# Performance work log

Hardware: AMD Instinct MI355X
Metric: run time of the kernel (lower is better)

## Reference

```python
import jax, jax.numpy as jnp
import numpy as np

V, SMAX, D, H, L, DFF, W = 32000, 1024, 1024, 16, 2, 4096, 256
HD = D // H
EPS = 1e-6


def setup_inputs() -> dict:
    key = jax.random.key(0)
    ks = jax.random.split(key, 20)
    s = lambda k, shape, scale=0.02: jax.random.normal(k, shape, dtype=jnp.float32) * scale
    return {
        "input_ids": jax.random.randint(ks[0], (2, SMAX), 0, V, dtype=jnp.int64),
        "emb": s(ks[1], (V, D)),
        "pos": s(ks[2], (SMAX, D)),
        "norm1_w": jnp.ones((L, D), jnp.float32),
        "norm2_w": jnp.ones((L, D), jnp.float32),
        "wq": s(ks[3], (L, D, D)), "bq": jnp.zeros((L, D), jnp.float32),
        "wk": s(ks[4], (L, D, D)), "bk": jnp.zeros((L, D), jnp.float32),
        "wv": s(ks[5], (L, D, D)), "bv": jnp.zeros((L, D), jnp.float32),
        "wo": s(ks[6], (L, D, D)), "bo": jnp.zeros((L, D), jnp.float32),
        "w1": s(ks[7], (L, D, DFF)), "b1": jnp.zeros((L, DFF), jnp.float32),
        "w2": s(ks[8], (L, DFF, D)), "b2": jnp.zeros((L, D), jnp.float32),
        "normf_w": jnp.ones((D,), jnp.float32),
    }


def rms(x, w):
    return x * jax.lax.rsqrt(jnp.mean(x * x, axis=-1, keepdims=True) + EPS) * w


def reference(input_ids, emb, pos, norm1_w, norm2_w, wq, bq, wk, bk, wv, bv,
              wo, bo, w1, b1, w2, b2, normf_w):
    B, S = input_ids.shape
    x = emb[input_ids] + pos[:S]  # [B,S,D]
    # sliding-window causal mask: attend to j with 0 <= i-j < W
    i = jnp.arange(S)[:, None]
    j = jnp.arange(S)[None, :]
    mask = (j <= i) & (i - j < W)  # [S,S]
    neg = jnp.asarray(-1e9, x.dtype)
    for l in range(L):
        h = rms(x, norm1_w[l])
        q = (h @ wq[l] + bq[l]).reshape(B, S, H, HD)
        k = (h @ wk[l] + bk[l]).reshape(B, S, H, HD)
        v = (h @ wv[l] + bv[l]).reshape(B, S, H, HD)
        scores = jnp.einsum('bqhd,bkhd->bhqk', q, k) / np.sqrt(HD).astype(np.float32)
        scores = jnp.where(mask[None, None], scores, neg)
        attn = jax.nn.softmax(scores, axis=-1)
        o = jnp.einsum('bhqk,bkhd->bqhd', attn, v).reshape(B, S, D)
        x = x + (o @ wo[l] + bo[l])
        h2 = rms(x, norm2_w[l])
        x = x + (jax.nn.gelu(h2 @ w1[l] + b1[l], approximate=False) @ w2[l] + b2[l])
    x = rms(x, normf_w)
    logits = x @ emb.T  # tied lm_head
    return logits
```

## Files before the change

kernel.cpp:

```cpp
#include <hip/hip_runtime.h>
#include <hip/hip_bf16.h>
#include <cstdint>

typedef __bf16 bf16;
typedef __bf16 bf16x8 __attribute__((ext_vector_type(8)));
typedef __bf16 bf16x4 __attribute__((ext_vector_type(4)));
typedef float  f32x4  __attribute__((ext_vector_type(4)));

constexpr int V_    = 32000;
constexpr int SMAX_ = 1024;
constexpr int D_    = 1024;
constexpr int H_    = 16;
constexpr int L_    = 2;
constexpr int DFF_  = 4096;
constexpr int WIN_  = 256;
constexpr int B_    = 2;
constexpr int M_    = B_ * SMAX_;

#define SBAR0_() __builtin_amdgcn_sched_barrier(0)
#define HWBAR_() { __builtin_amdgcn_s_barrier(); SBAR0_(); }
#define LGKM0_() { asm volatile("s_waitcnt lgkmcnt(0)" ::: "memory"); SBAR0_(); }
#define VM0_()   { asm volatile("s_waitcnt vmcnt(0)" ::: "memory"); SBAR0_(); }

__global__ __launch_bounds__(512, 1) void gemm_lm3(
    const bf16* __restrict__ A, const bf16* __restrict__ BT,
    float* __restrict__ outf, int Nn)
{
  constexpr int KK = 1024, NT = 16;
  __shared__ __align__(16) bf16 ldsA[2][16384];
  __shared__ __align__(16) bf16 ldsB[2][16384];

  const int t = threadIdx.x, lane = t & 63, w = t >> 6;
  const int l16 = lane & 15, lh = lane >> 4;
  const int wm = w >> 2, wn = w & 3;

  const int nloc = gridDim.x >> 3;
  const int wg = (blockIdx.x & 7) * nloc + (blockIdx.x >> 3);
  const long m0 = (long)(wg & 7) * 256;
  const long n0 = (long)(wg >> 3) * 256;

  auto STGA = [&](int c, int k0) {
    #pragma unroll
    for (int q = 0; q < 4; ++q) {
      int row = q * 64 + (t >> 3);
      int sl  = (t & 7) ^ (row & 7);
      const bf16* g = A + (m0 + row) * (long)KK + k0 + sl * 8;
      __builtin_amdgcn_global_load_lds(
          (const __attribute__((address_space(1))) uint32_t*)g,
          (__attribute__((address_space(3))) uint32_t*)(&ldsA[c][q * 4096 + t * 8]),
          16, 0, 0);
    }
  };
  auto STGB = [&](int c, int k0) {
    #pragma unroll
    for (int q = 0; q < 4; ++q) {
      int row = q * 64 + (t >> 3);
      int sl  = (t & 7) ^ (row & 7);
      const bf16* g = BT + (n0 + row) * (long)KK + k0 + sl * 8;
      __builtin_amdgcn_global_load_lds(
          (const __attribute__((address_space(1))) uint32_t*)g,
          (__attribute__((address_space(3))) uint32_t*)(&ldsB[c][q * 4096 + t * 8]),
          16, 0, 0);
    }
  };
  auto LDA = [&](int c, int mi, int ks) -> bf16x8 {
    int row = wm * 128 + mi * 16 + l16;
    int sl  = (ks * 4 + lh) ^ (row & 7);
    return *(const bf16x8*)(&ldsA[c][row * 64 + sl * 8]);
  };
  auto LDB = [&](int c, int ni, int ks) -> bf16x8 {
    int row = wn * 64 + ni * 16 + l16;
    int sl  = (ks * 4 + lh) ^ (row & 7);
    return *(const bf16x8*)(&ldsB[c][row * 64 + sl * 8]);
  };

  f32x4 acc[8][4] = {};
  bf16x8 a[8], b[4];

  STGA(0, 0); STGB(0, 0);
  int kNext = 64;

  for (int j = 0; j < NT; ++j) {
    const int c = j & 1;
    VM0_();
    HWBAR_();
    #pragma unroll
    for (int mi = 0; mi < 8; ++mi) a[mi] = LDA(c, mi, 0);
    #pragma unroll
    for (int ni = 0; ni < 4; ++ni) b[ni] = LDB(c, ni, 0);
    STGA(c ^ 1, kNext); STGB(c ^ 1, kNext);
    LGKM0_();
    __builtin_amdgcn_s_setprio(1);
    #pragma unroll
    for (int mi = 0; mi < 8; ++mi)
      #pragma unroll
      for (int ni = 0; ni < 4; ++ni)
        acc[mi][ni] = __builtin_amdgcn_mfma_f32_16x16x32_bf16(a[mi], b[ni], acc[mi][ni], 0, 0, 0);
    __builtin_amdgcn_s_setprio(0);
    HWBAR_();
    #pragma unroll
    for (int mi = 0; mi < 8; ++mi) a[mi] = LDA(c, mi, 1);
    #pragma unroll
    for (int ni = 0; ni < 4; ++ni) b[ni] = LDB(c, ni, 1);
    LGKM0_();
    __builtin_amdgcn_s_setprio(1);
    #pragma unroll
    for (int mi = 0; mi < 8; ++mi)
      #pragma unroll
      for (int ni = 0; ni < 4; ++ni)
        acc[mi][ni] = __builtin_amdgcn_mfma_f32_16x16x32_bf16(a[mi], b[ni], acc[mi][ni], 0, 0, 0);
    __builtin_amdgcn_s_setprio(0);
    kNext += 64; if (kNext == KK) kNext = 0;
  }

  asm volatile("s_waitcnt vmcnt(0) lgkmcnt(0)" ::: "memory");
  #pragma unroll
  for (int mi = 0; mi < 8; ++mi)
    #pragma unroll
    for (int ni = 0; ni < 4; ++ni)
      #pragma unroll
      for (int rr = 0; rr < 4; ++rr) {
        long row = m0 + wm * 128 + mi * 16 + lh * 4 + rr;
        long col = n0 + wn * 64 + ni * 16 + l16;
        outf[row * Nn + col] = acc[mi][ni][rr];
      }
}

template<int BM, int EPI>
__global__ __launch_bounds__(256) void gemm_l2(
    const bf16* __restrict__ A, const bf16* __restrict__ BT,
    const float* __restrict__ bias, float* __restrict__ resid,
    bf16* __restrict__ outb, float* __restrict__ outf,
    int Nn, int Kk, int nbyMask, int nbyShift)
{
  constexpr int MR = BM / 32;
  constexpr int CA = BM / 32;
  __shared__ __align__(16) bf16 ldsA[2][BM * 64];
  __shared__ __align__(16) bf16 ldsB[2][8192];

  const int t = threadIdx.x, lane = t & 63, w = t >> 6;
  const int l16 = lane & 15, lh = lane >> 4;
  const int wm = w >> 1, wn = w & 1;

  const int nwg = gridDim.x, bid = blockIdx.x;
  const int nloc = nwg >> 3;
  const int wg = (bid & 7) * nloc + (bid >> 3);
  const long m0 = (long)(wg & nbyMask) * BM;
  const long n0 = (long)(wg >> nbyShift) * 128;

  auto STGA = [&](int c, int k0) {
    #pragma unroll
    for (int q = 0; q < CA; ++q) {
      int row = q * 32 + (t >> 3);
      int sl  = (t & 7) ^ (row & 7);
      const bf16* g = A + (m0 + row) * (long)Kk + k0 + sl * 8;
      __builtin_amdgcn_global_load_lds(
          (const __attribute__((address_space(1))) uint32_t*)g,
          (__attribute__((address_space(3))) uint32_t*)(&ldsA[c][q * 2048 + t * 8]),
          16, 0, 0);
    }
  };
  auto STGB = [&](int c, int k0) {
    #pragma unroll
    for (int q = 0; q < 4; ++q) {
      int row = q * 32 + (t >> 3);
      int sl  = (t & 7) ^ (row & 7);
      const bf16* g = BT + (n0 + row) * (long)Kk + k0 + sl * 8;
      __builtin_amdgcn_global_load_lds(
          (const __attribute__((address_space(1))) uint32_t*)g,
          (__attribute__((address_space(3))) uint32_t*)(&ldsB[c][q * 2048 + t * 8]),
          16, 0, 0);
    }
  };
  auto LDA = [&](int c, int mi, int ks) -> bf16x8 {
    int row = wm * (BM / 2) + mi * 16 + l16;
    int sl  = (ks * 4 + lh) ^ (row & 7);
    return *(const bf16x8*)(&ldsA[c][row * 64 + sl * 8]);
  };
  auto LDB = [&](int c, int ni, int ks) -> bf16x8 {
    int row = wn * 64 + ni * 16 + l16;
    int sl  = (ks * 4 + lh) ^ (row & 7);
    return *(const bf16x8*)(&ldsB[c][row * 64 + sl * 8]);
  };

  f32x4 acc[MR][4] = {};
  bf16x8 a[MR], b[4];

  STGA(0, 0); STGB(0, 0);
  int kNext = 64;

  const int NT = Kk >> 6;
  for (int j = 0; j < NT; ++j) {
    const int c = j & 1;
    VM0_();
    HWBAR_();
    #pragma unroll
    for (int mi = 0; mi < MR; ++mi) a[mi] = LDA(c, mi, 0);
    #pragma unroll
    for (int ni = 0; ni < 4; ++ni) b[ni] = LDB(c, ni, 0);
    STGA(c ^ 1, kNext); STGB(c ^ 1, kNext);
    LGKM0_();
    __builtin_amdgcn_s_setprio(1);
    #pragma unroll
    for (int mi = 0; mi < MR; ++mi)
      #pragma unroll
      for (int ni = 0; ni < 4; ++ni)
        acc[mi][ni] = __builtin_amdgcn_mfma_f32_16x16x32_bf16(a[mi], b[ni], acc[mi][ni], 0, 0, 0);
    __builtin_amdgcn_s_setprio(0);
    HWBAR_();
    #pragma unroll
    for (int mi = 0; mi < MR; ++mi) a[mi] = LDA(c, mi, 1);
    #pragma unroll
    for (int ni = 0; ni < 4; ++ni) b[ni] = LDB(c, ni, 1);
    LGKM0_();
    __builtin_amdgcn_s_setprio(1);
    #pragma unroll
    for (int mi = 0; mi < MR; ++mi)
      #pragma unroll
      for (int ni = 0; ni < 4; ++ni)
        acc[mi][ni] = __builtin_amdgcn_mfma_f32_16x16x32_bf16(a[mi], b[ni], acc[mi][ni], 0, 0, 0);
    __builtin_amdgcn_s_setprio(0);
    kNext += 64; if (kNext == Kk) kNext = 0;
  }

  #pragma unroll
  for (int mi = 0; mi < MR; ++mi)
    #pragma unroll
    for (int ni = 0; ni < 4; ++ni)
      #pragma unroll
      for (int rr = 0; rr < 4; ++rr) {
        long row = m0 + wm * (BM / 2) + mi * 16 + lh * 4 + rr;
        long col = n0 + wn * 64 + ni * 16 + l16;
        float v = acc[mi][ni][rr];
        if (EPI == 0) {
          outb[row * Nn + col] = (bf16)(v + bias[col]);
        } else if (EPI == 1) {
          float xx = v + bias[col];
          outb[row * Nn + col] = (bf16)(0.5f * xx * (1.0f + erff(xx * 0.70710678118654752f)));
        } else if (EPI == 2) {
          resid[row * Nn + col] += v + bias[col];
        } else {
          outf[row * Nn + col] = v;
        }
      }
}

__global__ __launch_bounds__(256) void attn_swa(
    const bf16* __restrict__ qkv, bf16* __restrict__ o)
{
  constexpr int PADK = 72;
  constexpr int PADV = 40;
  __shared__ bf16 Qs[64 * PADK];
  __shared__ bf16 Ks[32 * PADK];
  __shared__ bf16 Vt[64 * PADV];
  __shared__ bf16 Ps[4][16 * PADV];

  const int bid = blockIdx.x;
  const int qb = bid & 15;
  const int h  = (bid >> 4) & 15;
  const int b  = bid >> 8;
  const int q0 = qb * 64;
  const int t = threadIdx.x, lane = t & 63, w = t >> 6;
  const int l16 = lane & 15, lh = lane >> 4;

  #pragma unroll
  for (int i = 0; i < 2; i++) {
    int e = t + i * 256;
    int row = e >> 3, cc = e & 7;
    uint4 g = *(const uint4*)(qkv + ((long)(b * SMAX_ + q0 + row)) * 3072 + h * 64 + cc * 8);
    *(uint4*)(Qs + row * PADK + cc * 8) = g;
  }
  __syncthreads();
  bf16x8 aq[2];
  const int qrow = w * 16 + l16;
  #pragma unroll
  for (int ks = 0; ks < 2; ks++)
    aq[ks] = *(const bf16x8*)(Qs + qrow * PADK + ks * 32 + lh * 8);

  float m_run[4], l_run[4];
  f32x4 oacc[4];
  #pragma unroll
  for (int rr = 0; rr < 4; rr++) { m_run[rr] = -1e30f; l_run[rr] = 0.0f; }
  #pragma unroll
  for (int n = 0; n < 4; n++) oacc[n] = (f32x4){0.f, 0.f, 0.f, 0.f};

  const int tlo = q0 - (WIN_ - 1);
  const int jlo = (tlo <= 0) ? 0 : (tlo & ~31);
  const int iq  = q0 + w * 16 + lh * 4;

  for (int j0 = jlo; j0 < q0 + 64; j0 += 32) {
    __syncthreads();
    {
      int row = t >> 3, cc = t & 7;
      long base = ((long)(b * SMAX_ + j0 + row)) * 3072 + h * 64 + cc * 8;
      uint4 gk = *(const uint4*)(qkv + base + 1024);
      *(uint4*)(Ks + row * PADK + cc * 8) = gk;
      bf16x8 vv = *(const bf16x8*)(qkv + base + 2048);
      #pragma unroll
      for (int j = 0; j < 8; j++)
        Vt[(cc * 8 + j) * PADV + row] = vv[j];
    }
    __syncthreads();

    f32x4 s[2] = {(f32x4){0.f,0.f,0.f,0.f}, (f32x4){0.f,0.f,0.f,0.f}};
    #pragma unroll
    for (int nt = 0; nt < 2; nt++)
      #pragma unroll
      for (int ks = 0; ks < 2; ks++) {
        bf16x8 bk = *(const bf16x8*)(Ks + (nt * 16 + l16) * PADK + ks * 32 + lh * 8);
        s[nt] = __builtin_amdgcn_mfma_f32_16x16x32_bf16(aq[ks], bk, s[nt], 0, 0, 0);
      }

    float sc[2][4];
    #pragma unroll
    for (int nt = 0; nt < 2; nt++)
      #pragma unroll
      for (int rr = 0; rr < 4; rr++) {
        int i = iq + rr;
        int j = j0 + nt * 16 + l16;
        float v = s[nt][rr] * 0.125f;
        bool ok = (j <= i) && (i - j < WIN_);
        sc[nt][rr] = ok ? v : -1e30f;
      }

    float pb[2][4], alpha[4];
    #pragma unroll
    for (int rr = 0; rr < 4; rr++) {
      float mt = fmaxf(sc[0][rr], sc[1][rr]);
      #pragma unroll
      for (int off = 1; off < 16; off <<= 1) mt = fmaxf(mt, __shfl_xor(mt, off, 64));
      float mn = fmaxf(m_run[rr], mt);
      float a = __expf(m_run[rr] - mn);
      m_run[rr] = mn; alpha[rr] = a;
      float p0 = __expf(sc[0][rr] - mn);
      float p1 = __expf(sc[1][rr] - mn);
      pb[0][rr] = p0; pb[1][rr] = p1;
      float ls = p0 + p1;
      #pragma unroll
      for (int off = 1; off < 16; off <<= 1) ls += __shfl_xor(ls, off, 64);
      l_run[rr] = l_run[rr] * a + ls;
    }
    #pragma unroll
    for (int n = 0; n < 4; n++)
      #pragma unroll
      for (int rr = 0; rr < 4; rr++) oacc[n][rr] *= alpha[rr];

    #pragma unroll
    for (int rr = 0; rr < 4; rr++) {
      int prow = lh * 4 + rr;
      Ps[w][prow * PADV + l16]      = (bf16)pb[0][rr];
      Ps[w][prow * PADV + 16 + l16] = (bf16)pb[1][rr];
    }
    __syncthreads();

    bf16x8 pa = *(const bf16x8*)(&Ps[w][l16 * PADV + lh * 8]);
    #pragma unroll
    for (int n = 0; n < 4; n++) {
      bf16x8 bv = *(const bf16x8*)(Vt + (n * 16 + l16) * PADV + lh * 8);
      oacc[n] = __builtin_amdgcn_mfma_f32_16x16x32_bf16(pa, bv, oacc[n], 0, 0, 0);
    }
  }

  #pragma unroll
  for (int rr = 0; rr < 4; rr++) {
    int i = iq + rr;
    float inv = 1.0f / l_run[rr];
    #pragma unroll
    for (int n = 0; n < 4; n++)
      o[((long)(b * SMAX_ + i)) * D_ + h * 64 + n * 16 + l16] = (bf16)(oacc[n][rr] * inv);
  }
}

__global__ __launch_bounds__(256) void transpose_cvt(
    const float* __restrict__ src, bf16* __restrict__ dst,
    int Kk, int Nn, long srcL, long dstL)
{
  __shared__ float tile[32][33];
  const int tx = threadIdx.x, ty = threadIdx.y;
  const long n0 = (long)blockIdx.x * 32, k0 = (long)blockIdx.y * 32;
  src += (long)blockIdx.z * srcL;
  dst += (long)blockIdx.z * dstL;
  #pragma unroll
  for (int i = 0; i < 4; i++)
    tile[ty + i * 8][tx] = src[(k0 + ty + i * 8) * Nn + n0 + tx];
  __syncthreads();
  #pragma unroll
  for (int i = 0; i < 4; i++)
    dst[(n0 + ty + i * 8) * Kk + k0 + tx] = (bf16)tile[tx][ty + i * 8];
}

__global__ __launch_bounds__(256) void cvt_bf16(
    const float* __restrict__ src, bf16* __restrict__ dst, long n4)
{
  long i = (long)blockIdx.x * 256 + threadIdx.x;
  if (i >= n4) return;
  float4 v = ((const float4*)src)[i];
  bf16x4 o; o[0] = (bf16)v.x; o[1] = (bf16)v.y; o[2] = (bf16)v.z; o[3] = (bf16)v.w;
  ((bf16x4*)dst)[i] = o;
}

__global__ __launch_bounds__(256) void pack_bqkv(
    const float* __restrict__ bq, const float* __restrict__ bk,
    const float* __restrict__ bv, float* __restrict__ out)
{
  int i = blockIdx.x * 256 + threadIdx.x;
  if (i >= L_ * 3072) return;
  int l = i / 3072, c = i % 3072;
  float v = (c < 1024) ? bq[l * 1024 + c]
          : (c < 2048) ? bk[l * 1024 + c - 1024]
                       : bv[l * 1024 + c - 2048];
  out[i] = v;
}

__global__ __launch_bounds__(256) void embed_k(
    const int* __restrict__ ids, const float* __restrict__ emb,
    const float* __restrict__ pos, float* __restrict__ x)
{
  const int m = blockIdx.x, t = threadIdx.x;
  const int id = ids[m];
  const int s = m & (SMAX_ - 1);
  float4 e = ((const float4*)(emb + (long)id * D_))[t];
  float4 p = ((const float4*)(pos + (long)s * D_))[t];
  float4 rr; rr.x = e.x + p.x; rr.y = e.y + p.y; rr.z = e.z + p.z; rr.w = e.w + p.w;
  ((float4*)(x + (long)m * D_))[t] = rr;
}

__global__ __launch_bounds__(256) void rmsnorm_k(
    const float* __restrict__ x, const float* __restrict__ wgt,
    bf16* __restrict__ out)
{
  __shared__ float red[4];
  const int m = blockIdx.x, t = threadIdx.x;
  float4 v = ((const float4*)(x + (long)m * D_))[t];
  float ss = v.x * v.x + v.y * v.y + v.z * v.z + v.w * v.w;
  #pragma unroll
  for (int off = 1; off < 64; off <<= 1) ss += __shfl_xor(ss, off, 64);
  const int lane = t & 63, w = t >> 6;
  if (lane == 0) red[w] = ss;
  __syncthreads();
  float tot = red[0] + red[1] + red[2] + red[3];
  float rs = rsqrtf(tot * (1.0f / D_) + 1e-6f);
  float4 g = ((const float4*)wgt)[t];
  bf16x4 o;
  o[0] = (bf16)(v.x * rs * g.x); o[1] = (bf16)(v.y * rs * g.y);
  o[2] = (bf16)(v.z * rs * g.z); o[3] = (bf16)(v.w * rs * g.w);
  ((bf16x4*)(out + (long)m * D_))[t] = o;
}

extern "C" void kernel_launch(void* const* d_in, const int* in_sizes, int n_in,
                              void* d_out, int out_size, void* d_ws, size_t ws_size,
                              hipStream_t stream)
{
  const int*   ids = (const int*)d_in[0];
  const float* emb = (const float*)d_in[1];
  const float* pos = (const float*)d_in[2];
  const float* n1w = (const float*)d_in[3];
  const float* n2w = (const float*)d_in[4];
  const float* wq  = (const float*)d_in[5];
  const float* bq  = (const float*)d_in[6];
  const float* wk  = (const float*)d_in[7];
  const float* bk  = (const float*)d_in[8];
  const float* wv  = (const float*)d_in[9];
  const float* bv  = (const float*)d_in[10];
  const float* wo  = (const float*)d_in[11];
  const float* bo  = (const float*)d_in[12];
  const float* w1  = (const float*)d_in[13];
  const float* b1  = (const float*)d_in[14];
  const float* w2  = (const float*)d_in[15];
  const float* b2  = (const float*)d_in[16];
  const float* nfw = (const float*)d_in[17];

  char* p = (char*)d_ws;
  auto alloc = [&](size_t bytes) {
    char* rr = p; p += (bytes + 255) & ~(size_t)255; return rr;
  };
  bf16*  wqkv_t = (bf16*) alloc((size_t)L_ * 3 * 1024 * 1024 * 2);
  bf16*  wo_t   = (bf16*) alloc((size_t)L_ * 1024 * 1024 * 2);
  bf16*  w1_t   = (bf16*) alloc((size_t)L_ * 4096 * 1024 * 2);
  bf16*  w2_t   = (bf16*) alloc((size_t)L_ * 1024 * 4096 * 2);
  bf16*  emb_bf = (bf16*) alloc((size_t)V_ * D_ * 2);
  float* bqkv   = (float*)alloc((size_t)L_ * 3072 * 4);
  float* x      = (float*)alloc((size_t)M_ * D_ * 4);
  bf16*  hbuf   = (bf16*) alloc((size_t)M_ * D_ * 2);
  bf16*  qkv    = (bf16*) alloc((size_t)M_ * 3072 * 2);
  bf16*  obuf   = (bf16*) alloc((size_t)M_ * D_ * 2);
  bf16*  ff     = (bf16*) alloc((size_t)M_ * DFF_ * 2);

  const dim3 b32(32, 8, 1);
  transpose_cvt<<<dim3(32, 32, L_),  b32, 0, stream>>>(wq, wqkv_t,                1024, 1024, 1024 * 1024, 3 * 1024 * 1024);
  transpose_cvt<<<dim3(32, 32, L_),  b32, 0, stream>>>(wk, wqkv_t + 1024 * 1024,  1024, 1024, 1024 * 1024, 3 * 1024 * 1024);
  transpose_cvt<<<dim3(32, 32, L_),  b32, 0, stream>>>(wv, wqkv_t + 2*1024*1024,  1024, 1024, 1024 * 1024, 3 * 1024 * 1024);
  transpose_cvt<<<dim3(32, 32, L_),  b32, 0, stream>>>(wo, wo_t,                  1024, 1024, 1024 * 1024, 1024 * 1024);
  transpose_cvt<<<dim3(128, 32, L_), b32, 0, stream>>>(w1, w1_t,                  1024, 4096, 1024 * 4096, 4096 * 1024);
  transpose_cvt<<<dim3(32, 128, L_), b32, 0, stream>>>(w2, w2_t,                  4096, 1024, 4096 * 1024, 1024 * 4096);
  cvt_bf16<<<32000, 256, 0, stream>>>(emb, emb_bf, (long)V_ * D_ / 4);
  pack_bqkv<<<24, 256, 0, stream>>>(bq, bk, bv, bqkv);
  embed_k<<<M_, 256, 0, stream>>>(ids, emb, pos, x);

  for (int l = 0; l < L_; l++) {
    rmsnorm_k<<<M_, 256, 0, stream>>>(x, n1w + l * D_, hbuf);
    gemm_l2<64, 0><<<dim3(32 * 24), 256, 0, stream>>>(
        hbuf, wqkv_t + (size_t)l * 3 * 1024 * 1024, bqkv + l * 3072,
        nullptr, qkv, nullptr, 3072, 1024, 31, 5);
    attn_swa<<<B_ * H_ * (SMAX_ / 64), 256, 0, stream>>>(qkv, obuf);
    gemm_l2<64, 2><<<dim3(32 * 8), 256, 0, stream>>>(
        obuf, wo_t + (size_t)l * 1024 * 1024, bo + l * D_,
        x, nullptr, nullptr, 1024, 1024, 31, 5);
    rmsnorm_k<<<M_, 256, 0, stream>>>(x, n2w + l * D_, hbuf);
    gemm_l2<128, 1><<<dim3(16 * 32), 256, 0, stream>>>(
        hbuf, w1_t + (size_t)l * 4096 * 1024, b1 + l * DFF_,
        nullptr, ff, nullptr, 4096, 1024, 15, 4);
    gemm_l2<64, 2><<<dim3(32 * 8), 256, 0, stream>>>(
        ff, w2_t + (size_t)l * 1024 * 4096, b2 + l * D_,
        x, nullptr, nullptr, 1024, 4096, 31, 5);
  }
  rmsnorm_k<<<M_, 256, 0, stream>>>(x, nfw, hbuf);
  gemm_lm3<<<dim3(8 * (V_ / 256)), 512, 0, stream>>>(
      hbuf, emb_bf, (float*)d_out, V_);
}
```

Before: 629.9 us.

## Triple-buffer B tiles and split LM-head GEMM into four staggered phases

Rewrites the LM-head GEMM main loop so the B operand uses three LDS buffers, prefetched two k-steps ahead, while A stays double-buffered. Each k-step is split into four MFMA phases, each loading only two B fragments and issuing part of the next global-to-LDS copies. The full vmcnt(0) wait becomes vmcnt(4), so loads stay in flight across iterations. This aims to hide global-load latency and cut B register pressure, at the cost of more barriers per step and extra LDS (96KB).

```diff
diff --git a/kernel.cpp b/kernel.cpp
--- a/kernel.cpp
+++ b/kernel.cpp
@@ -21,14 +21,15 @@
 #define HWBAR_() { __builtin_amdgcn_s_barrier(); SBAR0_(); }
 #define LGKM0_() { asm volatile("s_waitcnt lgkmcnt(0)" ::: "memory"); SBAR0_(); }
 #define VM0_()   { asm volatile("s_waitcnt vmcnt(0)" ::: "memory"); SBAR0_(); }
-
-__global__ __launch_bounds__(512, 1) void gemm_lm3(
+#define VM4_()   { asm volatile("s_waitcnt vmcnt(4)" ::: "memory"); SBAR0_(); }
+
+__global__ __launch_bounds__(512, 1) void gemm_lm4(
     const bf16* __restrict__ A, const bf16* __restrict__ BT,
     float* __restrict__ outf, int Nn)
 {
   constexpr int KK = 1024, NT = 16;
   __shared__ __align__(16) bf16 ldsA[2][16384];
-  __shared__ __align__(16) bf16 ldsB[2][16384];
+  __shared__ __align__(16) bf16 ldsB[3][16384];
 
   const int t = threadIdx.x, lane = t & 63, w = t >> 6;
   const int l16 = lane & 15, lh = lane >> 4;
@@ -39,29 +40,23 @@
   const long m0 = (long)(wg & 7) * 256;
   const long n0 = (long)(wg >> 3) * 256;
 
-  auto STGA = [&](int c, int k0) {
-    #pragma unroll
-    for (int q = 0; q < 4; ++q) {
-      int row = q * 64 + (t >> 3);
-      int sl  = (t & 7) ^ (row & 7);
-      const bf16* g = A + (m0 + row) * (long)KK + k0 + sl * 8;
-      __builtin_amdgcn_global_load_lds(
-          (const __attribute__((address_space(1))) uint32_t*)g,
-          (__attribute__((address_space(3))) uint32_t*)(&ldsA[c][q * 4096 + t * 8]),
-          16, 0, 0);
-    }
-  };
-  auto STGB = [&](int c, int k0) {
-    #pragma unroll
-    for (int q = 0; q < 4; ++q) {
-      int row = q * 64 + (t >> 3);
-      int sl  = (t & 7) ^ (row & 7);
-      const bf16* g = BT + (n0 + row) * (long)KK + k0 + sl * 8;
-      __builtin_amdgcn_global_load_lds(
-          (const __attribute__((address_space(1))) uint32_t*)g,
-          (__attribute__((address_space(3))) uint32_t*)(&ldsB[c][q * 4096 + t * 8]),
-          16, 0, 0);
-    }
+  auto SA = [&](int c, int k0, int q) {
+    int row = q * 64 + (t >> 3);
+    int sl  = (t & 7) ^ (row & 7);
+    const bf16* g = A + (m0 + row) * (long)KK + k0 + sl * 8;
+    __builtin_amdgcn_global_load_lds(
+        (const __attribute__((address_space(1))) uint32_t*)g,
+        (__attribute__((address_space(3))) uint32_t*)(&ldsA[c][q * 4096 + t * 8]),
+        16, 0, 0);
+  };
+  auto SB = [&](int c, int k0, int q) {
+    int row = q * 64 + (t >> 3);
+    int sl  = (t & 7) ^ (row & 7);
+    const bf16* g = BT + (n0 + row) * (long)KK + k0 + sl * 8;
+    __builtin_amdgcn_global_load_lds(
+        (const __attribute__((address_space(1))) uint32_t*)g,
+        (__attribute__((address_space(3))) uint32_t*)(&ldsB[c][q * 4096 + t * 8]),
+        16, 0, 0);
   };
   auto LDA = [&](int c, int mi, int ks) -> bf16x8 {
     int row = wm * 128 + mi * 16 + l16;
@@ -75,42 +70,69 @@
   };
 
   f32x4 acc[8][4] = {};
-  bf16x8 a[8], b[4];
-
-  STGA(0, 0); STGB(0, 0);
-  int kNext = 64;
+  bf16x8 a[8], b0, b1;
+
+  #pragma unroll
+  for (int q = 0; q < 4; ++q) SA(0, 0, q);
+  #pragma unroll
+  for (int q = 0; q < 4; ++q) SB(0, 0, q);
+  #pragma unroll
+  for (int q = 0; q < 4; ++q) SB(1, 64, q);
 
   for (int j = 0; j < NT; ++j) {
-    const int c = j & 1;
-    VM0_();
+    const int cA = j & 1, cAn = cA ^ 1;
+    const int cB = j % 3, cBn = (j + 2) % 3;
+    const int kA = ((j + 1) & (NT - 1)) * 64;
+    const int kB = ((j + 2) & (NT - 1)) * 64;
+    VM4_();
     HWBAR_();
     #pragma unroll
-    for (int mi = 0; mi < 8; ++mi) a[mi] = LDA(c, mi, 0);
-    #pragma unroll
-    for (int ni = 0; ni < 4; ++ni) b[ni] = LDB(c, ni, 0);
-    STGA(c ^ 1, kNext); STGB(c ^ 1, kNext);
+    for (int mi = 0; mi < 8; ++mi) a[mi] = LDA(cA, mi, 0);
+    b0 = LDB(cB, 0, 0); b1 = LDB(cB, 1, 0);
+    SA(cAn, kA, 0); SA(cAn, kA, 1);
     LGKM0_();
     __builtin_amdgcn_s_setprio(1);
     #pragma unroll
-    for (int mi = 0; mi < 8; ++mi)
-      #pragma unroll
-      for (int ni = 0; ni < 4; ++ni)
-        acc[mi][ni] = __builtin_amdgcn_mfma_f32_16x16x32_bf16(a[mi], b[ni], acc[mi][ni], 0, 0, 0);
+    for (int mi = 0; mi < 8; ++mi) {
+      acc[mi][0] = __builtin_amdgcn_mfma_f32_16x16x32_bf16(a[mi], b0, acc[mi][0], 0, 0, 0);
+      acc[mi][1] = __builtin_amdgcn_mfma_f32_16x16x32_bf16(a[mi], b1, acc[mi][1], 0, 0, 0);
+    }
     __builtin_amdgcn_s_setprio(0);
     HWBAR_();
-    #pragma unroll
-    for (int mi = 0; mi < 8; ++mi) a[mi] = LDA(c, mi, 1);
-    #pragma unroll
-    for (int ni = 0; ni < 4; ++ni) b[ni] = LDB(c, ni, 1);
+    b0 = LDB(cB, 2, 0); b1 = LDB(cB, 3, 0);
+    SA(cAn, kA, 2); SA(cAn, kA, 3);
     LGKM0_();
     __builtin_amdgcn_s_setprio(1);
     #pragma unroll
-    for (int mi = 0; mi < 8; ++mi)
-      #pragma unroll
-      for (int ni = 0; ni < 4; ++ni)
-        acc[mi][ni] = __builtin_amdgcn_mfma_f32_16x16x32_bf16(a[mi], b[ni], acc[mi][ni], 0, 0, 0);
+    for (int mi = 0; mi < 8; ++mi) {
+      acc[mi][2] = __builtin_amdgcn_mfma_f32_16x16x32_bf16(a[mi], b0, acc[mi][2], 0, 0, 0);
+      acc[mi][3] = __builtin_amdgcn_mfma_f32_16x16x32_bf16(a[mi], b1, acc[mi][3], 0, 0, 0);
+    }
     __builtin_amdgcn_s_setprio(0);
-    kNext += 64; if (kNext == KK) kNext = 0;
+    HWBAR_();
+    #pragma unroll
+    for (int mi = 0; mi < 8; ++mi) a[mi] = LDA(cA, mi, 1);
+    b0 = LDB(cB, 0, 1); b1 = LDB(cB, 1, 1);
+    SB(cBn, kB, 0); SB(cBn, kB, 1);
+    LGKM0_();
+    __builtin_amdgcn_s_setprio(1);
+    #pragma unroll
+    for (int mi = 0; mi < 8; ++mi) {
+      acc[mi][0] = __builtin_amdgcn_mfma_f32_16x16x32_bf16(a[mi], b0, acc[mi][0], 0, 0, 0);
+      acc[mi][1] = __builtin_amdgcn_mfma_f32_16x16x32_bf16(a[mi], b1, acc[mi][1], 0, 0, 0);
+    }
+    __builtin_amdgcn_s_setprio(0);
+    HWBAR_();
+    b0 = LDB(cB, 2, 1); b1 = LDB(cB, 3, 1);
+    SB(cBn, kB, 2); SB(cBn, kB, 3);
+    LGKM0_();
+    __builtin_amdgcn_s_setprio(1);
+    #pragma unroll
+    for (int mi = 0; mi < 8; ++mi) {
+      acc[mi][2] = __builtin_amdgcn_mfma_f32_16x16x32_bf16(a[mi], b0, acc[mi][2], 0, 0, 0);
+      acc[mi][3] = __builtin_amdgcn_mfma_f32_16x16x32_bf16(a[mi], b1, acc[mi][3], 0, 0, 0);
+    }
+    __builtin_amdgcn_s_setprio(0);
   }
 
   asm volatile("s_waitcnt vmcnt(0) lgkmcnt(0)" ::: "memory");
@@ -515,6 +537,6 @@
         x, nullptr, nullptr, 1024, 4096, 31, 5);
   }
   rmsnorm_k<<<M_, 256, 0, stream>>>(x, nfw, hbuf);
-  gemm_lm3<<<dim3(8 * (V_ / 256)), 512, 0, stream>>>(
+  gemm_lm4<<<dim3(8 * (V_ / 256)), 512, 0, stream>>>(
       hbuf, emb_bf, (float*)d_out, V_);
 }
```

New measurement: 670.7 us. 6.5% more time.
